# Optimization experiments

Hardware: AMD Instinct MI355X
Metric: run time of the kernel (lower is better)

Reference implementation:

```python
import jax, jax.numpy as jnp
import numpy as np

BETA = 1e-8
ALPHA = 0.5
CHOOSE_K = 128
MEMORY_SIZE = 65536
KEY_DIM = 256
BATCH = 1024


def _l2norm(x, axis=-1, eps=1e-12):
    return x / jnp.sqrt(jnp.sum(x * x, axis=axis, keepdims=True) + eps)


def setup_inputs() -> dict:
    key = jax.random.key(0)
    k1, k2, k3 = jax.random.split(key, 3)
    q = _l2norm(jax.random.normal(k1, (BATCH, KEY_DIM), dtype=jnp.float32))
    memory_key = _l2norm(jax.random.normal(k2, (MEMORY_SIZE, KEY_DIM), dtype=jnp.float32))
    # module init: hist[:] = 1e-5; add small random variation so topk is non-degenerate
    memory_hist = 1e-5 + 1e-3 * jax.random.uniform(k3, (MEMORY_SIZE,), dtype=jnp.float32)
    # module init: values = ones, second half zeroed
    memory_values = jnp.concatenate([
        jnp.ones((MEMORY_SIZE // 2,), dtype=jnp.float32),
        jnp.zeros((MEMORY_SIZE - MEMORY_SIZE // 2,), dtype=jnp.float32),
    ])
    return {"q": q, "memory_key": memory_key,
            "memory_hist": memory_hist, "memory_values": memory_values}


def reference(q, memory_key, memory_hist, memory_values):
    # obtain_topk over FULL memory: dense similarity [B, M]
    sims = jnp.matmul(q, memory_key.T)                      # [B, M]
    scores = jnp.exp(sims - 1.0) * (memory_hist + BETA)[None, :]
    _, k_idxs = jax.lax.top_k(scores, CHOOSE_K)             # [B, K]

    # gather reduced memory at topk indices
    red_keys = memory_key[k_idxs]                           # [B, K, D]
    red_hist = memory_hist[k_idxs] * ALPHA                  # [B, K]
    red_vals = memory_values[k_idxs]                        # [B, K]

    # posterior over the K gathered slots
    sim_k = jnp.einsum('bd,bkd->bk', q, red_keys)           # [B, K]
    joint = jnp.exp(sim_k - 1.0) * (red_hist + BETA)        # [B, K]
    posterior = joint / jnp.sum(joint, axis=1, keepdims=True)
    result = jnp.sum(posterior * red_vals, axis=1)          # [B]
    return result
```

## Files before the change

kernel.cpp:

```cpp
#include <hip/hip_runtime.h>

#define BATCH   1024
#define MSIZE   65536
#define KDIM    256
#define CHOOSEK 128
#define SELK    160
#define T0  156.0f
#define T1  160.0f
#define T2  164.0f
#define BETA    1e-8f
#define ALPHA   0.5f
#define KSC  425.0f
#define KOFF 7.2f

typedef short bf16x8 __attribute__((ext_vector_type(8)));
typedef float f32x4  __attribute__((ext_vector_type(4)));

__device__ inline unsigned int pack2bf(float a, float b) {
    unsigned int ua = __float_as_uint(a);
    unsigned int ub = __float_as_uint(b);
    ua += 0x7fffu + ((ua >> 16) & 1u);
    ub += 0x7fffu + ((ub >> 16) & 1u);
    return (ua >> 16) | (ub & 0xffff0000u);
}

#define GLD16(g, l) __builtin_amdgcn_global_load_lds( \
    (const __attribute__((address_space(1))) unsigned int*)(g), \
    (__attribute__((address_space(3))) unsigned int*)(l), 16, 0, 0)

__global__ __launch_bounds__(256)
void convert_kernel(const float* __restrict__ q, const float* __restrict__ key,
                    const float* __restrict__ hist,
                    unsigned short* __restrict__ qs, unsigned short* __restrict__ kb,
                    float* __restrict__ Ltab)
{
    const int bid = blockIdx.x, tid = threadIdx.x;
    if (bid < 8192) {
        const int off = bid * 256 + tid;
        const float4* s4 = (const float4*)key;
        float4 a = s4[off * 2], b = s4[off * 2 + 1];
        ((uint4*)kb)[off] = make_uint4(pack2bf(a.x, a.y), pack2bf(a.z, a.w),
                                       pack2bf(b.x, b.y), pack2bf(b.z, b.w));
    } else if (bid < 8320) {
        const int f = (bid - 8192) * 256 + tid;
        const int l = f & 63, j = (f >> 6) & 3, ks = (f >> 8) & 7;
        const int wmg = (f >> 11) & 3, bt = (f >> 13) & 3;
        const int r = bt * 256 + wmg * 64 + j * 16 + (l & 15);
        const int c = ks * 32 + (l >> 4) * 8;
        const float* src = q + (size_t)r * KDIM + c;
        float4 a = *(const float4*)src, b = *(const float4*)(src + 4);
        ((uint4*)qs)[f] = make_uint4(pack2bf(a.x, a.y), pack2bf(a.z, a.w),
                                     pack2bf(b.x, b.y), pack2bf(b.z, b.w));
    } else {
        const int n = (bid - 8320) * 256 + tid;
        Ltab[n] = (logf(hist[n] + BETA) + KOFF) * KSC;
    }
}

__global__ __launch_bounds__(512, 4)
void score_kernel(const unsigned short* __restrict__ qs,
                  const unsigned short* __restrict__ kb,
                  const float* __restrict__ Ltab,
                  unsigned long long* __restrict__ gmask)
{
    __shared__ __align__(16) unsigned short Bs[3][128 * 32];
    const int tid = threadIdx.x;
    const int bid = blockIdx.x;
    const int bt = (bid >> 3) & 3;
    const int b0 = bt * 256;
    const int n0 = ((bid & 7) + ((bid >> 5) << 3)) * 128;
    const int lane = tid & 63, wave = tid >> 6;
    const int wm = (wave >> 1) * 64, wn = (wave & 1) * 64;
    const int l15 = lane & 15, l4 = lane >> 4;
    const int wmg = wave >> 1;

    f32x4 acc[4][4] = {};

    const int srow = tid >> 2;
    const int seg  = (tid & 3) * 8;
    const unsigned short* gB = kb + (size_t)(n0 + srow) * KDIM + seg;
    const int lofs = srow * 32 + seg;

    const bf16x8* qw = (const bf16x8*)qs + (size_t)((bt * 4 + wmg) * 32) * 64 + lane;

    bf16x8 qf[2][4];

#define STAGE_B(st) GLD16(gB + (st) * 32, &Bs[(st) % 3][lofs])

#define STEP(s, WN) do {                                                          \
    asm volatile("s_waitcnt vmcnt(" #WN ")" ::: "memory");                        \
    __builtin_amdgcn_s_barrier();                                                 \
    asm volatile("" ::: "memory");                                                \
    if ((s) < 7) {                                                                \
        _Pragma("unroll")                                                         \
        for (int j = 0; j < 4; ++j)                                               \
            qf[((s) + 1) & 1][j] = qw[(((s) + 1) * 4 + j) * 64];                  \
    }                                                                             \
    if ((s) + 2 < 8) STAGE_B((s) + 2);                                            \
    bf16x8 kf[4];                                                                 \
    _Pragma("unroll")                                                             \
    for (int i = 0; i < 4; ++i)                                                   \
        kf[i] = *(const bf16x8*)(&Bs[(s) % 3][(wn + i * 16 + l15) * 32 + l4 * 8]);\
    __builtin_amdgcn_s_setprio(1);                                                \
    _Pragma("unroll")                                                             \
    for (int i = 0; i < 4; ++i)                                                   \
        _Pragma("unroll")                                                         \
        for (int j = 0; j < 4; ++j)                                               \
            acc[i][j] = __builtin_amdgcn_mfma_f32_16x16x32_bf16(kf[i], qf[(s) & 1][j], acc[i][j], 0, 0, 0); \
    __builtin_amdgcn_s_setprio(0);                                                \
} while (0)

#pragma unroll
    for (int j = 0; j < 4; ++j) qf[0][j] = qw[j * 64];
    STAGE_B(0); STAGE_B(1);

    STEP(0, 1); STEP(1, 1); STEP(2, 1); STEP(3, 1);
    STEP(4, 1); STEP(5, 1); STEP(6, 1); STEP(7, 0);

#undef STEP
#undef STAGE_B

    float4 Lv[4];
#pragma unroll
    for (int i = 0; i < 4; ++i)
        Lv[i] = *(const float4*)&Ltab[n0 + wn + i * 16 + l4 * 4];
#pragma unroll
    for (int j = 0; j < 4; ++j) {
        const int rb = b0 + wm + j * 16 + l15;
        unsigned int lo0 = 0, hi0 = 0, lo1 = 0, hi1 = 0, lo2 = 0, hi2 = 0;
#pragma unroll
        for (int i = 0; i < 4; ++i) {
            const float* lv = (const float*)&Lv[i];
            unsigned int n0b = 0, n1b = 0, n2b = 0;
#pragma unroll
            for (int reg = 0; reg < 4; ++reg) {
                float x = fmaf(acc[i][j][reg], KSC, lv[reg]);
                n0b |= (x >= T0 ? 1u : 0u) << reg;
                n1b |= (x >= T1 ? 1u : 0u) << reg;
                n2b |= (x >= T2 ? 1u : 0u) << reg;
            }
            const int sh = (i & 1) * 16 + l4 * 4;
            if (i < 2) { lo0 |= n0b << sh; lo1 |= n1b << sh; lo2 |= n2b << sh; }
            else       { hi0 |= n0b << sh; hi1 |= n1b << sh; hi2 |= n2b << sh; }
        }
        lo0 |= __shfl_xor(lo0, 16, 64); hi0 |= __shfl_xor(hi0, 16, 64);
        lo0 |= __shfl_xor(lo0, 32, 64); hi0 |= __shfl_xor(hi0, 32, 64);
        lo1 |= __shfl_xor(lo1, 16, 64); hi1 |= __shfl_xor(hi1, 16, 64);
        lo1 |= __shfl_xor(lo1, 32, 64); hi1 |= __shfl_xor(hi1, 32, 64);
        lo2 |= __shfl_xor(lo2, 16, 64); hi2 |= __shfl_xor(hi2, 16, 64);
        lo2 |= __shfl_xor(lo2, 32, 64); hi2 |= __shfl_xor(hi2, 32, 64);
        if (l4 == 0) {
            const size_t w = (size_t)rb * (MSIZE / 64) + ((n0 + wn) >> 6);
            const size_t lvl = (size_t)BATCH * (MSIZE / 64);
            gmask[w]           = ((unsigned long long)hi0 << 32) | lo0;
            gmask[w + lvl]     = ((unsigned long long)hi1 << 32) | lo1;
            gmask[w + 2 * lvl] = ((unsigned long long)hi2 << 32) | lo2;
        }
    }
}

__global__ __launch_bounds__(256, 4)
void select_kernel(const float* __restrict__ q,
                   const float* __restrict__ key,
                   const float* __restrict__ hist,
                   const float* __restrict__ vals,
                   const unsigned long long* __restrict__ gmask,
                   float* __restrict__ out)
{
    const int b   = blockIdx.x;
    const int tid = threadIdx.x;

    __shared__ __align__(16) float qs[KDIM];
    __shared__ int   scal[4];
    __shared__ int   cidx[1024];
    __shared__ float csc[1024], cjj[1024], cjv[1024];
    __shared__ float wred[8];

    qs[tid] = q[(size_t)b * KDIM + tid];
    const size_t lvl = (size_t)BATCH * (MSIZE / 64);
    const unsigned long long* gm = gmask + (size_t)b * (MSIZE / 64);

    if (tid < 4) scal[tid] = 0;
    __syncthreads();

    unsigned long long m0[4], m1[4], m2[4];
    int l0 = 0, l1 = 0, l2 = 0;
#pragma unroll
    for (int k = 0; k < 4; ++k) {
        m0[k] = gm[tid + k * 256];            l0 += __popcll(m0[k]);
        m1[k] = gm[tid + k * 256 + lvl];      l1 += __popcll(m1[k]);
        m2[k] = gm[tid + k * 256 + 2 * lvl];  l2 += __popcll(m2[k]);
    }
    { int r0 = l0, r1 = l1, r2 = l2;
#pragma unroll
      for (int off = 32; off > 0; off >>= 1) {
          r0 += __shfl_xor(r0, off, 64);
          r1 += __shfl_xor(r1, off, 64);
          r2 += __shfl_xor(r2, off, 64);
      }
      if ((tid & 63) == 0) {
          atomicAdd((unsigned int*)&scal[0], (unsigned int)r0);
          atomicAdd((unsigned int*)&scal[1], (unsigned int)r1);
          atomicAdd((unsigned int*)&scal[2], (unsigned int)r2);
      } }
    __syncthreads();
    const int c0 = scal[0], c1 = scal[1], c2 = scal[2];
    const int L = (c2 >= SELK && c2 <= 1024) ? 2
                : (c1 >= SELK && c1 <= 1024) ? 1 : 0;

    const int myc = (L == 2) ? l2 : (L == 1) ? l1 : l0;
    int base = atomicAdd(&scal[3], myc);
#define WALK(MW) do {                                                   \
    _Pragma("unroll")                                                   \
    for (int k = 0; k < 4; ++k) {                                       \
        unsigned long long m = MW[k];                                   \
        while (m) {                                                     \
            int bpos = __builtin_ctzll(m);                              \
            m &= m - 1;                                                 \
            if (base < 1024) cidx[base] = (tid + k * 256) * 64 + bpos;  \
            ++base;                                                     \
        }                                                               \
    }                                                                   \
} while (0)
    if (L == 2) WALK(m2); else if (L == 1) WALK(m1); else WALK(m0);
#undef WALK
    __syncthreads();
    const int ncand = min(scal[3], 1024);

    const int gid = tid >> 4, gll = tid & 15;
    const float4* q4 = (const float4*)qs;
    for (int i = gid; i < ncand; i += 16) {
        const int idx = cidx[i];
        const float4* kp = (const float4*)(key + (size_t)idx * KDIM);
        float p = 0.f;
#pragma unroll
        for (int u = 0; u < 4; ++u) {
            float4 kk = kp[gll * 4 + u];
            float4 qq = q4[gll * 4 + u];
            p += kk.x * qq.x + kk.y * qq.y + kk.z * qq.z + kk.w * qq.w;
        }
#pragma unroll
        for (int off = 1; off < 16; off <<= 1) p += __shfl_xor(p, off, 64);
        if (gll == 0) {
            float e = expf(p - 1.0f);
            float h = hist[idx];
            csc[i] = e * (h + BETA);
            float j = e * (ALPHA * h + BETA);
            cjj[i] = j;
            cjv[i] = j * vals[idx];
        }
    }
    __syncthreads();

    const int wave = tid >> 6, lane = tid & 63;
    float pn = 0.f, pd = 0.f;
    for (int i = tid; i < ncand; i += 256) {
        float si = csc[i]; int ii = cidx[i]; int rank = 0;
        for (int t = 0; t < ncand; ++t) {
            float st = csc[t];
            rank += (st > si || (st == si && cidx[t] < ii)) ? 1 : 0;
        }
        if (rank < CHOOSEK) { pn += cjv[i]; pd += cjj[i]; }
    }
#pragma unroll
    for (int off = 32; off > 0; off >>= 1) {
        pn += __shfl_xor(pn, off, 64);
        pd += __shfl_xor(pd, off, 64);
    }
    if (lane == 0) { wred[wave] = pn; wred[4 + wave] = pd; }
    __syncthreads();
    if (tid == 0) {
        float n = wred[0] + wred[1] + wred[2] + wred[3];
        float d = wred[4] + wred[5] + wred[6] + wred[7];
        out[b] = n / d;
    }
}

extern "C" void kernel_launch(void* const* d_in, const int* in_sizes, int n_in,
                              void* d_out, int out_size, void* d_ws, size_t ws_size,
                              hipStream_t stream)
{
    (void)in_sizes; (void)n_in; (void)out_size; (void)ws_size;
    const float* q    = (const float*)d_in[0];
    const float* key  = (const float*)d_in[1];
    const float* hist = (const float*)d_in[2];
    const float* vals = (const float*)d_in[3];
    float* out = (float*)d_out;

    unsigned short* kb = (unsigned short*)d_ws;
    unsigned short* qsw= (unsigned short*)((char*)d_ws + ((size_t)32 << 20));
    float*          Lt = (float*)((char*)d_ws + ((size_t)32 << 20) + (512 << 10));
    unsigned long long* gmask = (unsigned long long*)((char*)d_ws + ((size_t)33 << 20));

    convert_kernel<<<8576, 256, 0, stream>>>(q, key, hist, qsw, kb, Lt);
    score_kernel<<<2048, 512, 0, stream>>>(qsw, kb, Lt, gmask);
    select_kernel<<<BATCH, 256, 0, stream>>>(q, key, hist, vals, gmask, out);
}
```

Baseline: 186.9 us.

## Pre-swizzle keys into MFMA fragment layout and drop LDS staging in score kernel

The convert kernel now writes bf16 keys directly in per-lane MFMA fragment order, so the score kernel loads both operands straight from global memory into registers with double buffering. This removes the LDS staging, barriers and global_load_lds path. Tiles shrink to 128x128 with 256-thread blocks, which doubles the grid. The mask layout is transposed to level/word/batch order, and the select kernel now reads one level at a time starting from the tightest, falling back to lower levels only when the count is out of range. The trade-off is that each key tile is loaded by more blocks without LDS sharing, and the select kernel's loads become strided across the batch dimension.

```diff
diff --git a/kernel.cpp b/kernel.cpp
--- a/kernel.cpp
+++ b/kernel.cpp
@@ -12,6 +12,7 @@
 #define ALPHA   0.5f
 #define KSC  425.0f
 #define KOFF 7.2f
+#define LVLW ((size_t)1024 * 1024)
 
 typedef short bf16x8 __attribute__((ext_vector_type(8)));
 typedef float f32x4  __attribute__((ext_vector_type(4)));
@@ -24,28 +25,28 @@
     return (ua >> 16) | (ub & 0xffff0000u);
 }
 
-#define GLD16(g, l) __builtin_amdgcn_global_load_lds( \
-    (const __attribute__((address_space(1))) unsigned int*)(g), \
-    (__attribute__((address_space(3))) unsigned int*)(l), 16, 0, 0)
-
 __global__ __launch_bounds__(256)
 void convert_kernel(const float* __restrict__ q, const float* __restrict__ key,
                     const float* __restrict__ hist,
-                    unsigned short* __restrict__ qs, unsigned short* __restrict__ kb,
+                    unsigned short* __restrict__ qs, unsigned short* __restrict__ kbf,
                     float* __restrict__ Ltab)
 {
     const int bid = blockIdx.x, tid = threadIdx.x;
     if (bid < 8192) {
-        const int off = bid * 256 + tid;
-        const float4* s4 = (const float4*)key;
-        float4 a = s4[off * 2], b = s4[off * 2 + 1];
-        ((uint4*)kb)[off] = make_uint4(pack2bf(a.x, a.y), pack2bf(a.z, a.w),
-                                       pack2bf(b.x, b.y), pack2bf(b.z, b.w));
+        const int t = bid * 256 + tid;
+        const int l = t & 63, f = t >> 6;
+        const int i = f & 3, ks = (f >> 2) & 7, wnh = (f >> 5) & 1, nt = f >> 6;
+        const int row = nt * 128 + wnh * 64 + i * 16 + (l & 15);
+        const int col = ks * 32 + (l >> 4) * 8;
+        const float* src = key + (size_t)row * KDIM + col;
+        float4 a = *(const float4*)src, b = *(const float4*)(src + 4);
+        ((uint4*)kbf)[t] = make_uint4(pack2bf(a.x, a.y), pack2bf(a.z, a.w),
+                                      pack2bf(b.x, b.y), pack2bf(b.z, b.w));
     } else if (bid < 8320) {
         const int f = (bid - 8192) * 256 + tid;
         const int l = f & 63, j = (f >> 6) & 3, ks = (f >> 8) & 7;
-        const int wmg = (f >> 11) & 3, bt = (f >> 13) & 3;
-        const int r = bt * 256 + wmg * 64 + j * 16 + (l & 15);
+        const int wmg = (f >> 11) & 1, bt = f >> 12;
+        const int r = bt * 128 + wmg * 64 + j * 16 + (l & 15);
         const int c = ks * 32 + (l >> 4) * 8;
         const float* src = q + (size_t)r * KDIM + c;
         float4 a = *(const float4*)src, b = *(const float4*)(src + 4);
@@ -57,68 +58,49 @@
     }
 }
 
-__global__ __launch_bounds__(512, 4)
+__global__ __launch_bounds__(256)
 void score_kernel(const unsigned short* __restrict__ qs,
-                  const unsigned short* __restrict__ kb,
+                  const unsigned short* __restrict__ kbf,
                   const float* __restrict__ Ltab,
                   unsigned long long* __restrict__ gmask)
 {
-    __shared__ __align__(16) unsigned short Bs[3][128 * 32];
     const int tid = threadIdx.x;
     const int bid = blockIdx.x;
-    const int bt = (bid >> 3) & 3;
-    const int b0 = bt * 256;
-    const int n0 = ((bid & 7) + ((bid >> 5) << 3)) * 128;
+    const int bt = (bid >> 3) & 7;
+    const int b0 = bt * 128;
+    const int nt = (bid & 7) | ((bid >> 6) << 3);
+    const int n0 = nt * 128;
     const int lane = tid & 63, wave = tid >> 6;
     const int wm = (wave >> 1) * 64, wn = (wave & 1) * 64;
     const int l15 = lane & 15, l4 = lane >> 4;
-    const int wmg = wave >> 1;
 
     f32x4 acc[4][4] = {};
 
-    const int srow = tid >> 2;
-    const int seg  = (tid & 3) * 8;
-    const unsigned short* gB = kb + (size_t)(n0 + srow) * KDIM + seg;
-    const int lofs = srow * 32 + seg;
-
-    const bf16x8* qw = (const bf16x8*)qs + (size_t)((bt * 4 + wmg) * 32) * 64 + lane;
-
-    bf16x8 qf[2][4];
-
-#define STAGE_B(st) GLD16(gB + (st) * 32, &Bs[(st) % 3][lofs])
-
-#define STEP(s, WN) do {                                                          \
-    asm volatile("s_waitcnt vmcnt(" #WN ")" ::: "memory");                        \
-    __builtin_amdgcn_s_barrier();                                                 \
-    asm volatile("" ::: "memory");                                                \
-    if ((s) < 7) {                                                                \
-        _Pragma("unroll")                                                         \
-        for (int j = 0; j < 4; ++j)                                               \
-            qf[((s) + 1) & 1][j] = qw[(((s) + 1) * 4 + j) * 64];                  \
-    }                                                                             \
-    if ((s) + 2 < 8) STAGE_B((s) + 2);                                            \
-    bf16x8 kf[4];                                                                 \
-    _Pragma("unroll")                                                             \
-    for (int i = 0; i < 4; ++i)                                                   \
-        kf[i] = *(const bf16x8*)(&Bs[(s) % 3][(wn + i * 16 + l15) * 32 + l4 * 8]);\
-    __builtin_amdgcn_s_setprio(1);                                                \
-    _Pragma("unroll")                                                             \
-    for (int i = 0; i < 4; ++i)                                                   \
-        _Pragma("unroll")                                                         \
-        for (int j = 0; j < 4; ++j)                                               \
-            acc[i][j] = __builtin_amdgcn_mfma_f32_16x16x32_bf16(kf[i], qf[(s) & 1][j], acc[i][j], 0, 0, 0); \
-    __builtin_amdgcn_s_setprio(0);                                                \
-} while (0)
-
-#pragma unroll
-    for (int j = 0; j < 4; ++j) qf[0][j] = qw[j * 64];
-    STAGE_B(0); STAGE_B(1);
-
-    STEP(0, 1); STEP(1, 1); STEP(2, 1); STEP(3, 1);
-    STEP(4, 1); STEP(5, 1); STEP(6, 1); STEP(7, 0);
-
-#undef STEP
-#undef STAGE_B
+    const bf16x8* qw = (const bf16x8*)qs  + (size_t)((bt * 2 + (wave >> 1)) * 32) * 64 + lane;
+    const bf16x8* kw = (const bf16x8*)kbf + (size_t)((nt * 2 + (wave &  1)) * 32) * 64 + lane;
+
+    bf16x8 qf[2][4], kf[2][4];
+#pragma unroll
+    for (int j = 0; j < 4; ++j) { qf[0][j] = qw[j * 64]; kf[0][j] = kw[j * 64]; }
+
+#pragma unroll
+    for (int s = 0; s < 8; ++s) {
+        const int cur = s & 1;
+        if (s < 7) {
+#pragma unroll
+            for (int j = 0; j < 4; ++j) {
+                qf[cur ^ 1][j] = qw[((s + 1) * 4 + j) * 64];
+                kf[cur ^ 1][j] = kw[((s + 1) * 4 + j) * 64];
+            }
+        }
+        __builtin_amdgcn_s_setprio(1);
+#pragma unroll
+        for (int i = 0; i < 4; ++i)
+#pragma unroll
+            for (int j = 0; j < 4; ++j)
+                acc[i][j] = __builtin_amdgcn_mfma_f32_16x16x32_bf16(kf[cur][i], qf[cur][j], acc[i][j], 0, 0, 0);
+        __builtin_amdgcn_s_setprio(0);
+    }
 
     float4 Lv[4];
 #pragma unroll
@@ -150,11 +132,10 @@
         lo2 |= __shfl_xor(lo2, 16, 64); hi2 |= __shfl_xor(hi2, 16, 64);
         lo2 |= __shfl_xor(lo2, 32, 64); hi2 |= __shfl_xor(hi2, 32, 64);
         if (l4 == 0) {
-            const size_t w = (size_t)rb * (MSIZE / 64) + ((n0 + wn) >> 6);
-            const size_t lvl = (size_t)BATCH * (MSIZE / 64);
-            gmask[w]           = ((unsigned long long)hi0 << 32) | lo0;
-            gmask[w + lvl]     = ((unsigned long long)hi1 << 32) | lo1;
-            gmask[w + 2 * lvl] = ((unsigned long long)hi2 << 32) | lo2;
+            const size_t ofs = ((size_t)(nt * 2) + (wn >> 6)) * 1024 + rb;
+            gmask[ofs]            = ((unsigned long long)hi0 << 32) | lo0;
+            gmask[ofs + LVLW]     = ((unsigned long long)hi1 << 32) | lo1;
+            gmask[ofs + 2 * LVLW] = ((unsigned long long)hi2 << 32) | lo2;
         }
     }
 }
@@ -171,61 +152,51 @@
     const int tid = threadIdx.x;
 
     __shared__ __align__(16) float qs[KDIM];
-    __shared__ int   scal[4];
+    __shared__ int   scal[2];
     __shared__ int   cidx[1024];
     __shared__ float csc[1024], cjj[1024], cjv[1024];
     __shared__ float wred[8];
 
     qs[tid] = q[(size_t)b * KDIM + tid];
-    const size_t lvl = (size_t)BATCH * (MSIZE / 64);
-    const unsigned long long* gm = gmask + (size_t)b * (MSIZE / 64);
-
-    if (tid < 4) scal[tid] = 0;
-    __syncthreads();
-
-    unsigned long long m0[4], m1[4], m2[4];
-    int l0 = 0, l1 = 0, l2 = 0;
+    if (tid < 2) scal[tid] = 0;
+    __syncthreads();
+
+    unsigned long long mw[4];
+    int myc = 0;
+    int lvlsel = 2;
+    for (;;) {
+        myc = 0;
+#pragma unroll
+        for (int k = 0; k < 4; ++k) {
+            mw[k] = gmask[(size_t)lvlsel * LVLW + (size_t)(tid + k * 256) * 1024 + b];
+            myc += __popcll(mw[k]);
+        }
+        { int ws = myc;
+#pragma unroll
+          for (int off = 32; off > 0; off >>= 1) ws += __shfl_xor(ws, off, 64);
+          if ((tid & 63) == 0) atomicAdd((unsigned int*)&scal[0], (unsigned int)ws); }
+        __syncthreads();
+        const int c = scal[0];
+        __syncthreads();
+        if ((c >= SELK && c <= 1024) || lvlsel == 0) break;
+        if (tid == 0) scal[0] = 0;
+        __syncthreads();
+        --lvlsel;
+    }
+
+    int base = atomicAdd(&scal[1], myc);
 #pragma unroll
     for (int k = 0; k < 4; ++k) {
-        m0[k] = gm[tid + k * 256];            l0 += __popcll(m0[k]);
-        m1[k] = gm[tid + k * 256 + lvl];      l1 += __popcll(m1[k]);
-        m2[k] = gm[tid + k * 256 + 2 * lvl];  l2 += __popcll(m2[k]);
-    }
-    { int r0 = l0, r1 = l1, r2 = l2;
-#pragma unroll
-      for (int off = 32; off > 0; off >>= 1) {
-          r0 += __shfl_xor(r0, off, 64);
-          r1 += __shfl_xor(r1, off, 64);
-          r2 += __shfl_xor(r2, off, 64);
-      }
-      if ((tid & 63) == 0) {
-          atomicAdd((unsigned int*)&scal[0], (unsigned int)r0);
-          atomicAdd((unsigned int*)&scal[1], (unsigned int)r1);
-          atomicAdd((unsigned int*)&scal[2], (unsigned int)r2);
-      } }
-    __syncthreads();
-    const int c0 = scal[0], c1 = scal[1], c2 = scal[2];
-    const int L = (c2 >= SELK && c2 <= 1024) ? 2
-                : (c1 >= SELK && c1 <= 1024) ? 1 : 0;
-
-    const int myc = (L == 2) ? l2 : (L == 1) ? l1 : l0;
-    int base = atomicAdd(&scal[3], myc);
-#define WALK(MW) do {                                                   \
-    _Pragma("unroll")                                                   \
-    for (int k = 0; k < 4; ++k) {                                       \
-        unsigned long long m = MW[k];                                   \
-        while (m) {                                                     \
-            int bpos = __builtin_ctzll(m);                              \
-            m &= m - 1;                                                 \
-            if (base < 1024) cidx[base] = (tid + k * 256) * 64 + bpos;  \
-            ++base;                                                     \
-        }                                                               \
-    }                                                                   \
-} while (0)
-    if (L == 2) WALK(m2); else if (L == 1) WALK(m1); else WALK(m0);
-#undef WALK
-    __syncthreads();
-    const int ncand = min(scal[3], 1024);
+        unsigned long long m = mw[k];
+        while (m) {
+            int bpos = __builtin_ctzll(m);
+            m &= m - 1;
+            if (base < 1024) cidx[base] = (tid + k * 256) * 64 + bpos;
+            ++base;
+        }
+    }
+    __syncthreads();
+    const int ncand = min(scal[1], 1024);
 
     const int gid = tid >> 4, gll = tid & 15;
     const float4* q4 = (const float4*)qs;
@@ -287,12 +258,12 @@
     const float* vals = (const float*)d_in[3];
     float* out = (float*)d_out;
 
-    unsigned short* kb = (unsigned short*)d_ws;
+    unsigned short* kbf= (unsigned short*)d_ws;
     unsigned short* qsw= (unsigned short*)((char*)d_ws + ((size_t)32 << 20));
     float*          Lt = (float*)((char*)d_ws + ((size_t)32 << 20) + (512 << 10));
     unsigned long long* gmask = (unsigned long long*)((char*)d_ws + ((size_t)33 << 20));
 
-    convert_kernel<<<8576, 256, 0, stream>>>(q, key, hist, qsw, kb, Lt);
-    score_kernel<<<2048, 512, 0, stream>>>(qsw, kb, Lt, gmask);
+    convert_kernel<<<8576, 256, 0, stream>>>(q, key, hist, qsw, kbf, Lt);
+    score_kernel<<<4096, 256, 0, stream>>>(qsw, kbf, Lt, gmask);
     select_kernel<<<BATCH, 256, 0, stream>>>(q, key, hist, vals, gmask, out);
 }
```

After: 193.7 us. +3.7%, slower.
